# Optimization experiments

Measured on AMD Instinct MI355X. Metric: run time of the kernel, lower is better.

## Reference

```python
import jax, jax.numpy as jnp
import numpy as np
from jax import lax

B, TM1, NTS, NIN, H, D = 512, 64, 64, 63, 128, 128  # T-1 steps, encoder/decoder hidden
E = H  # encoder_hidden_size


def setup_inputs() -> dict:
    key = jax.random.key(0)
    ks = jax.random.split(key, 20)
    r = lambda k, s, sc=0.05: (jax.random.normal(k, s) * sc).astype(jnp.float32)
    return {
        "x": jax.random.normal(ks[0], (B, TM1, NTS), jnp.float32),
        # encoder input-attention linear: in = 2H + (T-1)
        "enc_attn_W": r(ks[1], (1, 2 * H + TM1)),
        "enc_attn_b": r(ks[2], (1,)),
        # encoder LSTM (input_size=NIN)
        "enc_Wih": r(ks[3], (4 * H, NIN)),
        "enc_Whh": r(ks[4], (4 * H, H)),
        "enc_bih": r(ks[5], (4 * H,)),
        "enc_bhh": r(ks[6], (4 * H,)),
        # decoder temporal-attention MLP: Linear(2D+E -> E), tanh, Linear(E -> 1)
        "dec_W1": r(ks[7], (E, 2 * D + E)),
        "dec_b1": r(ks[8], (E,)),
        "dec_W2": r(ks[9], (1, E)),
        "dec_b2": r(ks[10], (1,)),
        # decoder LSTM (input_size=out_feats=1)
        "dec_Wih": r(ks[11], (4 * D, 1)),
        "dec_Whh": r(ks[12], (4 * D, D)),
        "dec_bih": r(ks[13], (4 * D,)),
        "dec_bhh": r(ks[14], (4 * D,)),
        # fc: Linear(E+1 -> 1); original applies .normal_() (std=1) to fc weight
        "fc_W": jax.random.normal(ks[15], (1, E + 1), jnp.float32),
        "fc_b": r(ks[16], (1,)),
        # fc_final: Linear(D+E -> 1) (probabilistic=False)
        "fcf_W": r(ks[17], (1, D + E)),
        "fcf_b": r(ks[18], (1,)),
    }


def _lstm_step(xt, h, c, Wih, Whh, bih, bhh):
    # torch LSTM gate order: i, f, g, o
    g = xt @ Wih.T + h @ Whh.T + (bih + bhh)
    i, f, gg, o = jnp.split(g, 4, axis=-1)
    c = jax.nn.sigmoid(f) * c + jax.nn.sigmoid(i) * jnp.tanh(gg)
    h = jax.nn.sigmoid(o) * jnp.tanh(c)
    return h, c


def _forward(x, enc_attn_W, enc_attn_b, enc_Wih, enc_Whh, enc_bih, enc_bhh,
             dec_W1, dec_b1, dec_W2, dec_b2, dec_Wih, dec_Whh, dec_bih, dec_bhh,
             fc_W, fc_b, fcf_W, fcf_b):
    xin = x[:, :, 1:]            # (B, T-1, NIN) exogenous series
    y_hist = x[:, :, :1]         # (B, T-1, 1) target history
    z0 = jnp.zeros((x.shape[0], H), x.dtype)

    # ---- Encoder: input attention over features, LSTM over time ----
    # attn_linear([h, c, series_t]) = h@Wh + c@Wc + series@Wt + b (split the concat)
    Wh, Wc, Wt = enc_attn_W[0, :H], enc_attn_W[0, H:2 * H], enc_attn_W[0, 2 * H:]
    series_score = jnp.einsum('btn,t->bn', xin, Wt) + enc_attn_b[0]  # (B, NIN), const over steps

    def enc_step(carry, xt):  # xt: (B, NIN)
        h, c = carry
        score = h @ Wh + c @ Wc  # (B,)
        attn = jax.nn.softmax(score[:, None] + series_score, axis=1)  # (B, NIN)
        wi = attn * xt
        h, c = _lstm_step(wi, h, c, enc_Wih, enc_Whh, enc_bih, enc_bhh)
        return (h, c), h

    _, enc_hs = lax.scan(enc_step, (z0, z0), xin.transpose(1, 0, 2))
    input_encoded = enc_hs.transpose(1, 0, 2)  # (B, T-1, H)

    # ---- Decoder: temporal attention over encoded states, LSTM over time ----
    W1h, W1c, W1e = dec_W1[:, :D], dec_W1[:, D:2 * D], dec_W1[:, 2 * D:]
    enc_proj = jnp.einsum('bte,fe->btf', input_encoded, W1e) + dec_b1  # (B, T-1, E)

    def dec_step(carry, yt):  # yt: (B, 1)
        h, c, _ = carry
        z = jnp.tanh(enc_proj + (h @ W1h.T + c @ W1c.T)[:, None, :])   # (B, T-1, E)
        score = jnp.einsum('bte,e->bt', z, dec_W2[0]) + dec_b2[0]
        attn = jax.nn.softmax(score, axis=1)                            # (B, T-1)
        context = jnp.einsum('bt,bte->be', attn, input_encoded)         # (B, E)
        y_tilde = jnp.concatenate([context, yt], axis=1) @ fc_W.T + fc_b  # (B, 1)
        h, c = _lstm_step(y_tilde, h, c, dec_Wih, dec_Whh, dec_bih, dec_bhh)
        return (h, c, context), None

    (h, c, context), _ = lax.scan(
        dec_step, (z0, z0, jnp.zeros((x.shape[0], E), x.dtype)), y_hist.transpose(1, 0, 2))

    return jnp.concatenate([h, context], axis=1) @ fcf_W.T + fcf_b  # (B, 1)


def reference(x, enc_attn_W, enc_attn_b, enc_Wih, enc_Whh, enc_bih, enc_bhh,
              dec_W1, dec_b1, dec_W2, dec_b2, dec_Wih, dec_Whh, dec_bih, dec_bhh,
              fc_W, fc_b, fcf_W, fcf_b):
    return _forward(x, enc_attn_W, enc_attn_b, enc_Wih, enc_Whh, enc_bih, enc_bhh,
                    dec_W1, dec_b1, dec_W2, dec_b2, dec_Wih, dec_Whh, dec_bih, dec_bhh,
                    fc_W, fc_b, fcf_W, fcf_b)
```

## Files before the change

kernel.cpp:

```cpp
#include <hip/hip_runtime.h>


typedef _Float16 half2v __attribute__((ext_vector_type(2)));

#if defined(__has_builtin)
#if __has_builtin(__builtin_amdgcn_fdot2)
#define HAS_FDOT2 1
#endif
#endif

__device__ __forceinline__ float fast_rcp(float x) { return __builtin_amdgcn_rcpf(x); }
__device__ __forceinline__ float fast_tanh(float x) {
    return 1.f - 2.f * fast_rcp(1.f + __expf(2.f * x));
}
__device__ __forceinline__ float fast_sig(float x) { return fast_rcp(1.f + __expf(-x)); }

__device__ __forceinline__ unsigned int packh2(float a, float b) {
    half2v v; v.x = (_Float16)a; v.y = (_Float16)b;
    return __builtin_bit_cast(unsigned int, v);
}
__device__ __forceinline__ unsigned short packh1(float a) {
    return __builtin_bit_cast(unsigned short, (_Float16)a);
}
__device__ __forceinline__ float unph(unsigned short u) {
    return (float)__builtin_bit_cast(_Float16, u);
}
__device__ __forceinline__ float fdot2f(unsigned int w, unsigned int h, float acc) {
#if HAS_FDOT2
    return __builtin_amdgcn_fdot2(__builtin_bit_cast(half2v, w),
                                  __builtin_bit_cast(half2v, h), acc, false);
#else
    half2v wv = __builtin_bit_cast(half2v, w);
    half2v hv = __builtin_bit_cast(half2v, h);
    return acc + (float)wv.x * (float)hv.x + (float)wv.y * (float)hv.y;
#endif
}

#define NK2 56

__global__ __launch_bounds__(512) void darnn_fused(
    const float* __restrict__ x,
    const float* __restrict__ aW,  const float* __restrict__ ab,
    const float* __restrict__ eWih, const float* __restrict__ eWhh,
    const float* __restrict__ ebih, const float* __restrict__ ebhh,
    const float* __restrict__ dW1,  const float* __restrict__ db1,
    const float* __restrict__ W2,
    const float* __restrict__ dWih, const float* __restrict__ dWhh,
    const float* __restrict__ dbih, const float* __restrict__ dbhh,
    const float* __restrict__ fcW,  const float* __restrict__ fcb,
    const float* __restrict__ fcfW, const float* __restrict__ fcfb,
    float* __restrict__ out)
{
    const int b   = blockIdx.x;
    const int tid = threadIdx.x;
    const float* xb = x + b * 4096;

    __shared__ unsigned int   s_w16[NK2 * 512];
    __shared__ __align__(16) unsigned char s_rawB[16384];
    __shared__ unsigned short s_enc16[64 * 128];
    __shared__ float s_hc[256];
    __shared__ unsigned int s_hch[NK2];
    __shared__ float s_g[512];
    __shared__ float s_cp[512];
    __shared__ float s_hp[128];
    __shared__ float s_attn[64];
    __shared__ float s_sc[64];
    __shared__ float s_ctx[128];
    __shared__ float s_W2v[128];
    __shared__ float s_fc[130];
    __shared__ float s_y[64];
    __shared__ float s_yt;

    float* const s_x = (float*)s_rawB;
    unsigned short* const s_ep = (unsigned short*)s_rawB;

    if (tid < 128) s_W2v[tid] = W2[tid];
    if (tid < 130) s_fc[tid] = (tid < 129) ? fcW[tid] : fcb[0];
    if (tid < 64)  s_y[tid] = xb[tid * 64];

    {
        float wtail[16];
#pragma unroll
        for (int k2 = 0; k2 < NK2; ++k2) {
            float2 wv = *(const float2*)&eWhh[tid * 128 + 2 * k2];
            s_w16[k2 * 512 + tid] = packh2(wv.x, wv.y);
        }
#pragma unroll
        for (int k = 0; k < 16; ++k) wtail[k] = eWhh[tid * 128 + 112 + k];

#pragma unroll
        for (int i = tid; i < 4096; i += 512)
            s_x[i] = ((i & 63) != 63) ? xb[i + 1] : 0.f;

        float wih[64];
        for (int n = 0; n < 63; ++n) wih[n] = eWih[tid * 63 + n];
        wih[63] = 0.f;
        const float bias = ebih[tid] + ebhh[tid];

        if (tid < 128) s_hc[tid] = 0.f;
        if (tid < NK2) s_hch[tid] = 0u;
        __syncthreads();

        if (tid < 64) {
            float sc = -1e30f;
            if (tid < 63) {
                sc = ab[0];
                for (int t = 0; t < 64; ++t) sc += s_x[t * 64 + tid] * aW[256 + t];
            }
            float m = sc;
#pragma unroll
            for (int off = 32; off; off >>= 1) m = fmaxf(m, __shfl_xor(m, off));
            float e = (tid < 63) ? __expf(sc - m) : 0.f;
            float s = e;
#pragma unroll
            for (int off = 32; off; off >>= 1) s += __shfl_xor(s, off);
            s_attn[tid] = e / s;
        }
        __syncthreads();

#pragma unroll
        for (int n = 0; n < 64; ++n) wih[n] *= s_attn[n];

        float xa;
        {
            float a0 = 0.f, a1 = 0.f, a2 = 0.f, a3 = 0.f;
#pragma unroll
            for (int n = 0; n < 64; n += 4) {
                float4 v = *(const float4*)&s_x[n];
                a0 += wih[n]   * v.x; a1 += wih[n+1] * v.y;
                a2 += wih[n+2] * v.z; a3 += wih[n+3] * v.w;
            }
            xa = (a0 + a1) + (a2 + a3);
        }
        float c = 0.f;

        for (int t = 0; t < 64; ++t) {
            float a0 = bias + xa, a1 = 0.f, a2 = 0.f, a3 = 0.f;
#pragma unroll
            for (int k2 = 0; k2 < NK2; k2 += 4) {
                a0 = fdot2f(s_w16[(k2+0)*512 + tid], s_hch[k2+0], a0);
                a1 = fdot2f(s_w16[(k2+1)*512 + tid], s_hch[k2+1], a1);
                a2 = fdot2f(s_w16[(k2+2)*512 + tid], s_hch[k2+2], a2);
                a3 = fdot2f(s_w16[(k2+3)*512 + tid], s_hch[k2+3], a3);
            }
#pragma unroll
            for (int k = 0; k < 16; k += 4) {
                float4 v = *(const float4*)&s_hc[112 + k];
                a0 += wtail[k]   * v.x; a1 += wtail[k+1] * v.y;
                a2 += wtail[k+2] * v.z; a3 += wtail[k+3] * v.w;
            }
            const float acc = (a0 + a1) + (a2 + a3);
            const int q = tid >> 7;
            s_g[tid] = (q == 2) ? fast_tanh(acc) : fast_sig(acc);
            __syncthreads();
            if (tid < 128) {
                c = s_g[128 + tid] * c + s_g[tid] * s_g[256 + tid];
                float h = s_g[384 + tid] * fast_tanh(c);
                s_hc[tid] = h;
                s_enc16[t * 128 + tid] = packh1(h);
                float hx = __shfl_xor(h, 1);
                if (!(tid & 1) && tid < 112) s_hch[tid >> 1] = packh2(h, hx);
            }
            if (t < 63) {
                float b0 = 0.f, b1 = 0.f, b2 = 0.f, b3 = 0.f;
#pragma unroll
                for (int n = 0; n < 64; n += 4) {
                    float4 v = *(const float4*)&s_x[(t + 1) * 64 + n];
                    b0 += wih[n]   * v.x; b1 += wih[n+1] * v.y;
                    b2 += wih[n+2] * v.z; b3 += wih[n+3] * v.w;
                }
                xa = (b0 + b1) + (b2 + b3);
            }
            __syncthreads();
        }
    }

    {
        const int f = tid & 127, tq = tid >> 7;
        float acc[16];
        const float b1 = db1[f];
#pragma unroll
        for (int i = 0; i < 16; ++i) acc[i] = b1;
        const float* w1e = dW1 + f * 384 + 256;
        for (int e0 = 0; e0 < 128; e0 += 8) {
            float4 wa = *(const float4*)&w1e[e0];
            float4 wb = *(const float4*)&w1e[e0 + 4];
            const unsigned int wp0 = packh2(wa.x, wa.y), wp1 = packh2(wa.z, wa.w);
            const unsigned int wp2 = packh2(wb.x, wb.y), wp3 = packh2(wb.z, wb.w);
#pragma unroll
            for (int i = 0; i < 16; ++i) {
                const unsigned int* er =
                    (const unsigned int*)&s_enc16[(tq * 16 + i) * 128 + e0];
                float t0 = fdot2f(wp0, er[0], acc[i]);
                t0 = fdot2f(wp1, er[1], t0);
                t0 = fdot2f(wp2, er[2], t0);
                acc[i] = fdot2f(wp3, er[3], t0);
            }
        }
        __syncthreads();
#pragma unroll
        for (int i = 0; i < 16; ++i)
            s_ep[(tq * 16 + i) * 128 + f] = packh1(acc[i]);
    }

    {
        float wtail[16];
#pragma unroll
        for (int k2 = 0; k2 < NK2; ++k2) {
            float2 wv = *(const float2*)&dWhh[tid * 128 + 2 * k2];
            s_w16[k2 * 512 + tid] = packh2(wv.x, wv.y);
        }
#pragma unroll
        for (int k = 0; k < 16; ++k) wtail[k] = dWhh[tid * 128 + 112 + k];
        const float bias  = dbih[tid] + dbhh[tid];
        const float wih_s = dWih[tid];

        const int f4 = tid >> 2, qq = tid & 3, qq2 = (tid & 3) * 2;
        float w1[64];
#pragma unroll
        for (int j = 0; j < 16; ++j) {
            const int cj = (j + qq2) & 15;
#pragma unroll
            for (int rr = 0; rr < 4; ++rr)
                w1[4*j + rr] = dW1[f4 * 384 + qq * 64 + cj * 4 + rr];
        }
        const int tp = tid >> 3, p = tid & 7;
        if (tid < 256) s_hc[tid] = 0.f;
        if (tid < NK2) s_hch[tid] = 0u;
        float c = 0.f;
        __syncthreads();

        for (int t = 0; t < 64; ++t) {
            {
                float a0 = 0.f, a1 = 0.f, a2 = 0.f, a3 = 0.f;
#pragma unroll
                for (int j = 0; j < 16; ++j) {
                    const int cj = (j + qq2) & 15;
                    float4 v = *(const float4*)&s_hc[qq * 64 + cj * 4];
                    a0 += w1[4*j]   * v.x; a1 += w1[4*j+1] * v.y;
                    a2 += w1[4*j+2] * v.z; a3 += w1[4*j+3] * v.w;
                }
                float a = (a0 + a1) + (a2 + a3);
                a += __shfl_xor(a, 1);
                a += __shfl_xor(a, 2);
                if (qq == 0) s_hp[f4] = a;
            }
            __syncthreads();
            {
                float a = 0.f;
#pragma unroll
                for (int cc = 0; cc < 4; ++cc) {
                    const int cj = (cc + tp) & 3;
                    const unsigned int* e2 =
                        (const unsigned int*)&s_ep[tp * 128 + p * 16 + cj * 4];
                    const half2v ea = __builtin_bit_cast(half2v, e2[0]);
                    const half2v eb = __builtin_bit_cast(half2v, e2[1]);
                    float4 hv = *(const float4*)&s_hp [p * 16 + cj * 4];
                    float4 wv = *(const float4*)&s_W2v[p * 16 + cj * 4];
                    a += wv.x * fast_tanh((float)ea.x + hv.x);
                    a += wv.y * fast_tanh((float)ea.y + hv.y);
                    a += wv.z * fast_tanh((float)eb.x + hv.z);
                    a += wv.w * fast_tanh((float)eb.y + hv.w);
                }
                a += __shfl_xor(a, 1);
                a += __shfl_xor(a, 2);
                a += __shfl_xor(a, 4);
                if (p == 0) s_sc[tp] = a;
            }
            __syncthreads();
            if (tid < 64) {
                float sc = s_sc[tid];
                float m = sc;
#pragma unroll
                for (int off = 32; off; off >>= 1) m = fmaxf(m, __shfl_xor(m, off));
                float e = __expf(sc - m);
                float s = e;
#pragma unroll
                for (int off = 32; off; off >>= 1) s += __shfl_xor(s, off);
                s_sc[tid] = e / s;
            }
            __syncthreads();
            {
                const int e = tid & 127, q2 = tid >> 7;
                float a0 = 0.f, a1 = 0.f;
#pragma unroll
                for (int i = 0; i < 16; i += 2) {
                    a0 += s_sc[q2*16 + i]   * unph(s_enc16[(q2*16 + i)   * 128 + e]);
                    a1 += s_sc[q2*16 + i+1] * unph(s_enc16[(q2*16 + i+1) * 128 + e]);
                }
                s_cp[tid] = a0 + a1;
            }
            __syncthreads();
            if (tid < 64) {
                const float clo = s_cp[tid]       + s_cp[128 + tid]
                                + s_cp[256 + tid] + s_cp[384 + tid];
                const float chi = s_cp[64 + tid]  + s_cp[192 + tid]
                                + s_cp[320 + tid] + s_cp[448 + tid];
                s_ctx[tid]      = clo;
                s_ctx[64 + tid] = chi;
                float a = clo * s_fc[tid] + chi * s_fc[64 + tid];
#pragma unroll
                for (int off = 32; off; off >>= 1) a += __shfl_xor(a, off);
                if (tid == 0) s_yt = a + s_y[t] * s_fc[128] + s_fc[129];
            }
            float a_hh;
            {
                float a0 = bias, a1 = 0.f, a2 = 0.f, a3 = 0.f;
#pragma unroll
                for (int k2 = 0; k2 < NK2; k2 += 4) {
                    a0 = fdot2f(s_w16[(k2+0)*512 + tid], s_hch[k2+0], a0);
                    a1 = fdot2f(s_w16[(k2+1)*512 + tid], s_hch[k2+1], a1);
                    a2 = fdot2f(s_w16[(k2+2)*512 + tid], s_hch[k2+2], a2);
                    a3 = fdot2f(s_w16[(k2+3)*512 + tid], s_hch[k2+3], a3);
                }
#pragma unroll
                for (int k = 0; k < 16; k += 4) {
                    float4 v = *(const float4*)&s_hc[112 + k];
                    a0 += wtail[k]   * v.x; a1 += wtail[k+1] * v.y;
                    a2 += wtail[k+2] * v.z; a3 += wtail[k+3] * v.w;
                }
                a_hh = (a0 + a1) + (a2 + a3);
            }
            __syncthreads();
            {
                const float acc = a_hh + s_yt * wih_s;
                const int q = tid >> 7;
                s_g[tid] = (q == 2) ? fast_tanh(acc) : fast_sig(acc);
            }
            __syncthreads();
            if (tid < 128) {
                c = s_g[128 + tid] * c + s_g[tid] * s_g[256 + tid];
                float h = s_g[384 + tid] * fast_tanh(c);
                s_hc[tid]       = h;
                s_hc[128 + tid] = c;
                float hx = __shfl_xor(h, 1);
                if (!(tid & 1) && tid < 112) s_hch[tid >> 1] = packh2(h, hx);
            }
            __syncthreads();
        }
    }

    if (tid < 64) {
        float a = s_hc[tid]       * fcfW[tid]
                + s_hc[64 + tid]  * fcfW[64 + tid]
                + s_ctx[tid]      * fcfW[128 + tid]
                + s_ctx[64 + tid] * fcfW[192 + tid];
#pragma unroll
        for (int off = 32; off; off >>= 1) a += __shfl_xor(a, off);
        if (tid == 0) out[blockIdx.x] = a + fcfb[0];
    }
}

extern "C" void kernel_launch(void* const* d_in, const int* in_sizes, int n_in,
                              void* d_out, int out_size, void* d_ws, size_t ws_size,
                              hipStream_t stream) {
    const float* x      = (const float*)d_in[0];
    const float* aW     = (const float*)d_in[1];
    const float* ab     = (const float*)d_in[2];
    const float* eWih   = (const float*)d_in[3];
    const float* eWhh   = (const float*)d_in[4];
    const float* ebih   = (const float*)d_in[5];
    const float* ebhh   = (const float*)d_in[6];
    const float* dW1    = (const float*)d_in[7];
    const float* db1    = (const float*)d_in[8];
    const float* W2     = (const float*)d_in[9];
    const float* dWih   = (const float*)d_in[11];
    const float* dWhh   = (const float*)d_in[12];
    const float* dbih   = (const float*)d_in[13];
    const float* dbhh   = (const float*)d_in[14];
    const float* fcW    = (const float*)d_in[15];
    const float* fcb    = (const float*)d_in[16];
    const float* fcfW   = (const float*)d_in[17];
    const float* fcfb   = (const float*)d_in[18];
    float* out = (float*)d_out;

    darnn_fused<<<dim3(512), dim3(512), 0, stream>>>(
        x, aW, ab, eWih, eWhh, ebih, ebhh, dW1, db1, W2,
        dWih, dWhh, dbih, dbhh, fcW, fcb, fcfW, fcfb, out);
}
```

Baseline: 733.1 us.

## Keep recurrent weights in fp16 registers and pack inputs and state as half2

The first 96 columns of each LSTM hidden weight row now live in registers as packed fp16, and only the 32-column tail stays in LDS, so most of the per-step shared-memory weight reads go away. The exogenous inputs, the input weights and the decoder attention h/c state are all packed to half2, and their dot products use fdot2 instead of fp32 FMAs. The hidden state is read with 128-bit LDS vector loads. This raises register pressure and lowers precision, since the inputs and the cell state are now fp16.

```diff
diff --git a/kernel.cpp b/kernel.cpp
--- a/kernel.cpp
+++ b/kernel.cpp
@@ -2,6 +2,7 @@
 
 
 typedef _Float16 half2v __attribute__((ext_vector_type(2)));
+typedef unsigned int uint;
 
 #if defined(__has_builtin)
 #if __has_builtin(__builtin_amdgcn_fdot2)
@@ -15,9 +16,9 @@
 }
 __device__ __forceinline__ float fast_sig(float x) { return fast_rcp(1.f + __expf(-x)); }
 
-__device__ __forceinline__ unsigned int packh2(float a, float b) {
+__device__ __forceinline__ uint packh2(float a, float b) {
     half2v v; v.x = (_Float16)a; v.y = (_Float16)b;
-    return __builtin_bit_cast(unsigned int, v);
+    return __builtin_bit_cast(uint, v);
 }
 __device__ __forceinline__ unsigned short packh1(float a) {
     return __builtin_bit_cast(unsigned short, (_Float16)a);
@@ -25,7 +26,7 @@
 __device__ __forceinline__ float unph(unsigned short u) {
     return (float)__builtin_bit_cast(_Float16, u);
 }
-__device__ __forceinline__ float fdot2f(unsigned int w, unsigned int h, float acc) {
+__device__ __forceinline__ float fdot2f(uint w, uint h, float acc) {
 #if HAS_FDOT2
     return __builtin_amdgcn_fdot2(__builtin_bit_cast(half2v, w),
                                   __builtin_bit_cast(half2v, h), acc, false);
@@ -35,8 +36,6 @@
     return acc + (float)wv.x * (float)hv.x + (float)wv.y * (float)hv.y;
 #endif
 }
-
-#define NK2 56
 
 __global__ __launch_bounds__(512) void darnn_fused(
     const float* __restrict__ x,
@@ -55,14 +54,14 @@
     const int tid = threadIdx.x;
     const float* xb = x + b * 4096;
 
-    __shared__ unsigned int   s_w16[NK2 * 512];
-    __shared__ __align__(16) unsigned char s_rawB[16384];
-    __shared__ unsigned short s_enc16[64 * 128];
-    __shared__ float s_hc[256];
-    __shared__ unsigned int s_hch[NK2];
+    __shared__ __align__(16) uint s_wt[16 * 512];
+    __shared__ __align__(16) unsigned short s_enc16[64*128];
+    __shared__ __align__(16) uint u[64 * 64];
+    __shared__ __align__(16) uint s_hch[128];
     __shared__ float s_g[512];
     __shared__ float s_cp[512];
     __shared__ float s_hp[128];
+    __shared__ float s_hcf[128];
     __shared__ float s_attn[64];
     __shared__ float s_sc[64];
     __shared__ float s_ctx[128];
@@ -71,64 +70,76 @@
     __shared__ float s_y[64];
     __shared__ float s_yt;
 
-    float* const s_x = (float*)s_rawB;
-    unsigned short* const s_ep = (unsigned short*)s_rawB;
-
-    if (tid < 128) s_W2v[tid] = W2[tid];
-    if (tid < 130) s_fc[tid] = (tid < 129) ? fcW[tid] : fcb[0];
-    if (tid < 64)  s_y[tid] = xb[tid * 64];
-
+    uint whh16[48];
+
+    uint wih16[32];
+    float bias;
     {
-        float wtail[16];
-#pragma unroll
-        for (int k2 = 0; k2 < NK2; ++k2) {
-            float2 wv = *(const float2*)&eWhh[tid * 128 + 2 * k2];
-            s_w16[k2 * 512 + tid] = packh2(wv.x, wv.y);
-        }
-#pragma unroll
-        for (int k = 0; k < 16; ++k) wtail[k] = eWhh[tid * 128 + 112 + k];
-
-#pragma unroll
-        for (int i = tid; i < 4096; i += 512)
-            s_x[i] = ((i & 63) != 63) ? xb[i + 1] : 0.f;
-
-        float wih[64];
-        for (int n = 0; n < 63; ++n) wih[n] = eWih[tid * 63 + n];
-        wih[63] = 0.f;
-        const float bias = ebih[tid] + ebhh[tid];
-
-        if (tid < 128) s_hc[tid] = 0.f;
-        if (tid < NK2) s_hch[tid] = 0u;
-        __syncthreads();
-
-        if (tid < 64) {
-            float sc = -1e30f;
-            if (tid < 63) {
-                sc = ab[0];
-                for (int t = 0; t < 64; ++t) sc += s_x[t * 64 + tid] * aW[256 + t];
-            }
-            float m = sc;
-#pragma unroll
-            for (int off = 32; off; off >>= 1) m = fmaxf(m, __shfl_xor(m, off));
-            float e = (tid < 63) ? __expf(sc - m) : 0.f;
-            float s = e;
-#pragma unroll
-            for (int off = 32; off; off >>= 1) s += __shfl_xor(s, off);
-            s_attn[tid] = e / s;
-        }
-        __syncthreads();
-
-#pragma unroll
-        for (int n = 0; n < 64; ++n) wih[n] *= s_attn[n];
-
+#pragma unroll
+        for (int k = 0; k < 4; ++k) {
+            const int i = tid + 512 * k;
+            const int t = i >> 5, n2 = i & 31;
+            const float lo = xb[t * 64 + 2 * n2 + 1];
+            const float hi = (n2 < 31) ? xb[t * 64 + 2 * n2 + 2] : 0.f;
+            u[i] = packh2(lo, hi);
+        }
+        if (tid < 64)  s_y[tid] = xb[tid * 64];
+        if (tid < 128) s_W2v[tid] = W2[tid];
+        if (tid < 130) s_fc[tid] = (tid < 129) ? fcW[tid] : fcb[0];
+        if (tid < 128) s_hch[tid] = 0u;
+#pragma unroll
+        for (int j = 0; j < 48; ++j)
+            whh16[j] = packh2(eWhh[tid * 128 + 2 * j], eWhh[tid * 128 + 2 * j + 1]);
+#pragma unroll
+        for (int j = 0; j < 16; ++j)
+            s_wt[j * 512 + tid] = packh2(eWhh[tid * 128 + 96 + 2 * j],
+                                         eWhh[tid * 128 + 97 + 2 * j]);
+#pragma unroll
+        for (int j = 0; j < 32; ++j) {
+            const float lo = eWih[tid * 63 + 2 * j];
+            const float hi = (2 * j + 1 < 63) ? eWih[tid * 63 + 2 * j + 1] : 0.f;
+            wih16[j] = packh2(lo, hi);
+        }
+        bias = ebih[tid] + ebhh[tid];
+    }
+    __syncthreads();
+
+    if (tid < 64) {
+        const unsigned short* u16 = (const unsigned short*)u;
+        float sc = -1e30f;
+        if (tid < 63) {
+            sc = ab[0];
+            for (int t = 0; t < 64; ++t) sc += unph(u16[t * 64 + tid]) * aW[256 + t];
+        }
+        float m = sc;
+#pragma unroll
+        for (int off = 32; off; off >>= 1) m = fmaxf(m, __shfl_xor(m, off));
+        float e = (tid < 63) ? __expf(sc - m) : 0.f;
+        float s = e;
+#pragma unroll
+        for (int off = 32; off; off >>= 1) s += __shfl_xor(s, off);
+        s_attn[tid] = e / s;
+    }
+    __syncthreads();
+
+#pragma unroll
+    for (int j = 0; j < 32; ++j) {
+        half2v w = __builtin_bit_cast(half2v, wih16[j]);
+        wih16[j] = packh2((float)w.x * s_attn[2 * j], (float)w.y * s_attn[2 * j + 1]);
+    }
+
+    {
         float xa;
         {
+            const uint4* xv = (const uint4*)&u[0];
             float a0 = 0.f, a1 = 0.f, a2 = 0.f, a3 = 0.f;
 #pragma unroll
-            for (int n = 0; n < 64; n += 4) {
-                float4 v = *(const float4*)&s_x[n];
-                a0 += wih[n]   * v.x; a1 += wih[n+1] * v.y;
-                a2 += wih[n+2] * v.z; a3 += wih[n+3] * v.w;
+            for (int q = 0; q < 8; ++q) {
+                uint4 v = xv[q];
+                a0 = fdot2f(wih16[4*q+0], v.x, a0);
+                a1 = fdot2f(wih16[4*q+1], v.y, a1);
+                a2 = fdot2f(wih16[4*q+2], v.z, a2);
+                a3 = fdot2f(wih16[4*q+3], v.w, a3);
             }
             xa = (a0 + a1) + (a2 + a3);
         }
@@ -137,17 +148,20 @@
         for (int t = 0; t < 64; ++t) {
             float a0 = bias + xa, a1 = 0.f, a2 = 0.f, a3 = 0.f;
 #pragma unroll
-            for (int k2 = 0; k2 < NK2; k2 += 4) {
-                a0 = fdot2f(s_w16[(k2+0)*512 + tid], s_hch[k2+0], a0);
-                a1 = fdot2f(s_w16[(k2+1)*512 + tid], s_hch[k2+1], a1);
-                a2 = fdot2f(s_w16[(k2+2)*512 + tid], s_hch[k2+2], a2);
-                a3 = fdot2f(s_w16[(k2+3)*512 + tid], s_hch[k2+3], a3);
-            }
-#pragma unroll
-            for (int k = 0; k < 16; k += 4) {
-                float4 v = *(const float4*)&s_hc[112 + k];
-                a0 += wtail[k]   * v.x; a1 += wtail[k+1] * v.y;
-                a2 += wtail[k+2] * v.z; a3 += wtail[k+3] * v.w;
+            for (int q = 0; q < 12; ++q) {
+                uint4 hv = *(const uint4*)&s_hch[4 * q];
+                a0 = fdot2f(whh16[4*q+0], hv.x, a0);
+                a1 = fdot2f(whh16[4*q+1], hv.y, a1);
+                a2 = fdot2f(whh16[4*q+2], hv.z, a2);
+                a3 = fdot2f(whh16[4*q+3], hv.w, a3);
+            }
+#pragma unroll
+            for (int q = 0; q < 4; ++q) {
+                uint4 hv = *(const uint4*)&s_hch[48 + 4 * q];
+                a0 = fdot2f(s_wt[(4*q+0)*512 + tid], hv.x, a0);
+                a1 = fdot2f(s_wt[(4*q+1)*512 + tid], hv.y, a1);
+                a2 = fdot2f(s_wt[(4*q+2)*512 + tid], hv.z, a2);
+                a3 = fdot2f(s_wt[(4*q+3)*512 + tid], hv.w, a3);
             }
             const float acc = (a0 + a1) + (a2 + a3);
             const int q = tid >> 7;
@@ -156,18 +170,20 @@
             if (tid < 128) {
                 c = s_g[128 + tid] * c + s_g[tid] * s_g[256 + tid];
                 float h = s_g[384 + tid] * fast_tanh(c);
-                s_hc[tid] = h;
                 s_enc16[t * 128 + tid] = packh1(h);
                 float hx = __shfl_xor(h, 1);
-                if (!(tid & 1) && tid < 112) s_hch[tid >> 1] = packh2(h, hx);
+                if (!(tid & 1)) s_hch[tid >> 1] = packh2(h, hx);
             }
             if (t < 63) {
+                const uint4* xv = (const uint4*)&u[(t + 1) * 32];
                 float b0 = 0.f, b1 = 0.f, b2 = 0.f, b3 = 0.f;
 #pragma unroll
-                for (int n = 0; n < 64; n += 4) {
-                    float4 v = *(const float4*)&s_x[(t + 1) * 64 + n];
-                    b0 += wih[n]   * v.x; b1 += wih[n+1] * v.y;
-                    b2 += wih[n+2] * v.z; b3 += wih[n+3] * v.w;
+                for (int q = 0; q < 8; ++q) {
+                    uint4 v = xv[q];
+                    b0 = fdot2f(wih16[4*q+0], v.x, b0);
+                    b1 = fdot2f(wih16[4*q+1], v.y, b1);
+                    b2 = fdot2f(wih16[4*q+2], v.z, b2);
+                    b3 = fdot2f(wih16[4*q+3], v.w, b3);
                 }
                 xa = (b0 + b1) + (b2 + b3);
             }
@@ -185,60 +201,60 @@
         for (int e0 = 0; e0 < 128; e0 += 8) {
             float4 wa = *(const float4*)&w1e[e0];
             float4 wb = *(const float4*)&w1e[e0 + 4];
-            const unsigned int wp0 = packh2(wa.x, wa.y), wp1 = packh2(wa.z, wa.w);
-            const unsigned int wp2 = packh2(wb.x, wb.y), wp3 = packh2(wb.z, wb.w);
+            const uint wp0 = packh2(wa.x, wa.y), wp1 = packh2(wa.z, wa.w);
+            const uint wp2 = packh2(wb.x, wb.y), wp3 = packh2(wb.z, wb.w);
 #pragma unroll
             for (int i = 0; i < 16; ++i) {
-                const unsigned int* er =
-                    (const unsigned int*)&s_enc16[(tq * 16 + i) * 128 + e0];
+                const uint* er = (const uint*)&s_enc16[(tq * 16 + i) * 128 + e0];
                 float t0 = fdot2f(wp0, er[0], acc[i]);
                 t0 = fdot2f(wp1, er[1], t0);
                 t0 = fdot2f(wp2, er[2], t0);
                 acc[i] = fdot2f(wp3, er[3], t0);
             }
         }
-        __syncthreads();
+        unsigned short* ep16 = (unsigned short*)u;
 #pragma unroll
         for (int i = 0; i < 16; ++i)
-            s_ep[(tq * 16 + i) * 128 + f] = packh1(acc[i]);
-    }
-
+            ep16[(tq * 16 + i) * 128 + f] = packh1(acc[i]);
+    }
+
+    uint w1p[32];
+    float bias_d, wih_s;
+    const int f4 = tid >> 2, qq = tid & 3;
+    const int tp = tid >> 3, p = tid & 7;
     {
-        float wtail[16];
-#pragma unroll
-        for (int k2 = 0; k2 < NK2; ++k2) {
-            float2 wv = *(const float2*)&dWhh[tid * 128 + 2 * k2];
-            s_w16[k2 * 512 + tid] = packh2(wv.x, wv.y);
-        }
-#pragma unroll
-        for (int k = 0; k < 16; ++k) wtail[k] = dWhh[tid * 128 + 112 + k];
-        const float bias  = dbih[tid] + dbhh[tid];
-        const float wih_s = dWih[tid];
-
-        const int f4 = tid >> 2, qq = tid & 3, qq2 = (tid & 3) * 2;
-        float w1[64];
-#pragma unroll
-        for (int j = 0; j < 16; ++j) {
-            const int cj = (j + qq2) & 15;
-#pragma unroll
-            for (int rr = 0; rr < 4; ++rr)
-                w1[4*j + rr] = dW1[f4 * 384 + qq * 64 + cj * 4 + rr];
-        }
-        const int tp = tid >> 3, p = tid & 7;
-        if (tid < 256) s_hc[tid] = 0.f;
-        if (tid < NK2) s_hch[tid] = 0u;
+#pragma unroll
+        for (int j = 0; j < 48; ++j)
+            whh16[j] = packh2(dWhh[tid * 128 + 2 * j], dWhh[tid * 128 + 2 * j + 1]);
+#pragma unroll
+        for (int j = 0; j < 16; ++j)
+            s_wt[j * 512 + tid] = packh2(dWhh[tid * 128 + 96 + 2 * j],
+                                         dWhh[tid * 128 + 97 + 2 * j]);
+#pragma unroll
+        for (int j = 0; j < 32; ++j) {
+            const int cj = (j + 8 * qq) & 31;
+            w1p[j] = packh2(dW1[f4 * 384 + qq * 64 + 2 * cj],
+                            dW1[f4 * 384 + qq * 64 + 2 * cj + 1]);
+        }
+        bias_d = dbih[tid] + dbhh[tid];
+        wih_s  = dWih[tid];
+        if (tid < 128) s_hch[tid] = 0u;
+    }
+    __syncthreads();
+
+    {
         float c = 0.f;
-        __syncthreads();
 
         for (int t = 0; t < 64; ++t) {
             {
                 float a0 = 0.f, a1 = 0.f, a2 = 0.f, a3 = 0.f;
 #pragma unroll
-                for (int j = 0; j < 16; ++j) {
-                    const int cj = (j + qq2) & 15;
-                    float4 v = *(const float4*)&s_hc[qq * 64 + cj * 4];
-                    a0 += w1[4*j]   * v.x; a1 += w1[4*j+1] * v.y;
-                    a2 += w1[4*j+2] * v.z; a3 += w1[4*j+3] * v.w;
+                for (int j = 0; j < 32; j += 4) {
+                    const int r0 = (j + 8 * qq) & 31;
+                    a0 = fdot2f(w1p[j+0], s_hch[qq * 32 + r0], a0);
+                    a1 = fdot2f(w1p[j+1], s_hch[qq * 32 + ((j + 1 + 8*qq) & 31)], a1);
+                    a2 = fdot2f(w1p[j+2], s_hch[qq * 32 + ((j + 2 + 8*qq) & 31)], a2);
+                    a3 = fdot2f(w1p[j+3], s_hch[qq * 32 + ((j + 3 + 8*qq) & 31)], a3);
                 }
                 float a = (a0 + a1) + (a2 + a3);
                 a += __shfl_xor(a, 1);
@@ -251,8 +267,7 @@
 #pragma unroll
                 for (int cc = 0; cc < 4; ++cc) {
                     const int cj = (cc + tp) & 3;
-                    const unsigned int* e2 =
-                        (const unsigned int*)&s_ep[tp * 128 + p * 16 + cj * 4];
+                    const uint* e2 = &u[tp * 64 + p * 8 + cj * 2];
                     const half2v ea = __builtin_bit_cast(half2v, e2[0]);
                     const half2v eb = __builtin_bit_cast(half2v, e2[1]);
                     float4 hv = *(const float4*)&s_hp [p * 16 + cj * 4];
@@ -305,19 +320,22 @@
             }
             float a_hh;
             {
-                float a0 = bias, a1 = 0.f, a2 = 0.f, a3 = 0.f;
-#pragma unroll
-                for (int k2 = 0; k2 < NK2; k2 += 4) {
-                    a0 = fdot2f(s_w16[(k2+0)*512 + tid], s_hch[k2+0], a0);
-                    a1 = fdot2f(s_w16[(k2+1)*512 + tid], s_hch[k2+1], a1);
-                    a2 = fdot2f(s_w16[(k2+2)*512 + tid], s_hch[k2+2], a2);
-                    a3 = fdot2f(s_w16[(k2+3)*512 + tid], s_hch[k2+3], a3);
-                }
-#pragma unroll
-                for (int k = 0; k < 16; k += 4) {
-                    float4 v = *(const float4*)&s_hc[112 + k];
-                    a0 += wtail[k]   * v.x; a1 += wtail[k+1] * v.y;
-                    a2 += wtail[k+2] * v.z; a3 += wtail[k+3] * v.w;
+                float a0 = bias_d, a1 = 0.f, a2 = 0.f, a3 = 0.f;
+#pragma unroll
+                for (int q = 0; q < 12; ++q) {
+                    uint4 hv = *(const uint4*)&s_hch[4 * q];
+                    a0 = fdot2f(whh16[4*q+0], hv.x, a0);
+                    a1 = fdot2f(whh16[4*q+1], hv.y, a1);
+                    a2 = fdot2f(whh16[4*q+2], hv.z, a2);
+                    a3 = fdot2f(whh16[4*q+3], hv.w, a3);
+                }
+#pragma unroll
+                for (int q = 0; q < 4; ++q) {
+                    uint4 hv = *(const uint4*)&s_hch[48 + 4 * q];
+                    a0 = fdot2f(s_wt[(4*q+0)*512 + tid], hv.x, a0);
+                    a1 = fdot2f(s_wt[(4*q+1)*512 + tid], hv.y, a1);
+                    a2 = fdot2f(s_wt[(4*q+2)*512 + tid], hv.z, a2);
+                    a3 = fdot2f(s_wt[(4*q+3)*512 + tid], hv.w, a3);
                 }
                 a_hh = (a0 + a1) + (a2 + a3);
             }
@@ -331,18 +349,21 @@
             if (tid < 128) {
                 c = s_g[128 + tid] * c + s_g[tid] * s_g[256 + tid];
                 float h = s_g[384 + tid] * fast_tanh(c);
-                s_hc[tid]       = h;
-                s_hc[128 + tid] = c;
+                s_hcf[tid] = h;
                 float hx = __shfl_xor(h, 1);
-                if (!(tid & 1) && tid < 112) s_hch[tid >> 1] = packh2(h, hx);
+                float cx = __shfl_xor(c, 1);
+                if (!(tid & 1)) {
+                    s_hch[tid >> 1]        = packh2(h, hx);
+                    s_hch[64 + (tid >> 1)] = packh2(c, cx);
+                }
             }
             __syncthreads();
         }
     }
 
     if (tid < 64) {
-        float a = s_hc[tid]       * fcfW[tid]
-                + s_hc[64 + tid]  * fcfW[64 + tid]
+        float a = s_hcf[tid]      * fcfW[tid]
+                + s_hcf[64 + tid] * fcfW[64 + tid]
                 + s_ctx[tid]      * fcfW[128 + tid]
                 + s_ctx[64 + tid] * fcfW[192 + tid];
 #pragma unroll
```

Result: faster. 635.6 us (-13.3%).
